# Optimization experiments

Measured on AMD Instinct MI355X. Metric: run time of the kernel, lower is better.

Reference implementation:

```python
import jax, jax.numpy as jnp
import numpy as np

B, N, E, D, NS, H = 32, 4096, 256, 256, 8, 256
N_ITERS, N_SH, N_MESH, MESH_LR = 3, 5, 4, 5.0

def layer_norm(x, scale, bias, eps=1e-5):
    m = jnp.mean(x, axis=-1, keepdims=True)
    v = jnp.var(x, axis=-1, keepdims=True)
    return (x - m) / jnp.sqrt(v + eps) * scale + bias

def sinkhorn(C, a, b, u=None, v=None, n_iters=N_SH):
    # log-domain Sinkhorn with marginals a [B,N], b [B,S]; C [B,N,S]
    log_a, log_b = jnp.log(a), jnp.log(b)
    if u is None:
        u = jnp.zeros_like(a)
    if v is None:
        v = jnp.zeros_like(b)
    K = -C
    for _ in range(n_iters):
        u = log_a - jax.nn.logsumexp(K + v[:, None, :], axis=-1)
        v = log_b - jax.nn.logsumexp(K + u[:, :, None], axis=-2)
    attn = jnp.exp(K + u[:, :, None] + v[:, None, :])
    return attn, u, v

def minimize_entropy_of_sinkhorn(C0, a, b, mesh_lr=MESH_LR, n_mesh=N_MESH):
    # MESH: gradient-descend the cost matrix to minimize entropy of the transport plan
    def ent(C):
        attn, _, _ = sinkhorn(C, a, b)
        return -jnp.sum(attn * jnp.log(attn + 1e-8))
    C = C0
    for _ in range(n_mesh):
        C = C - mesh_lr * jax.grad(ent)(C)
    _, u, v = sinkhorn(C, a, b)
    return C, u, v

def gru_cell(x, h, Wih, Whh, bih, bhh):
    # torch.nn.GRUCell math, gate order (r, z, n)
    gi = x @ Wih.T + bih
    gh = h @ Whh.T + bhh
    ir, iz, inn = jnp.split(gi, 3, axis=-1)
    hr, hz, hn = jnp.split(gh, 3, axis=-1)
    r = jax.nn.sigmoid(ir + hr)
    z = jax.nn.sigmoid(iz + hz)
    n = jnp.tanh(inn + r * hn)
    return (1.0 - z) * n + z * h

def setup_inputs():
    key = jax.random.key(0)
    ks = jax.random.split(key, 16)
    s = 0.02
    return {
        "inputs": jax.random.normal(ks[0], (B, N, E), jnp.float32),
        "slots_init": jax.random.normal(ks[1], (B, NS, D), jnp.float32),
        "ln_in_s": jnp.ones((E,), jnp.float32), "ln_in_b": jnp.zeros((E,), jnp.float32),
        "ln_sl_s": jnp.ones((D,), jnp.float32), "ln_sl_b": jnp.zeros((D,), jnp.float32),
        "ln_mlp_s": jnp.ones((D,), jnp.float32), "ln_mlp_b": jnp.zeros((D,), jnp.float32),
        "Wq": jax.random.normal(ks[2], (D, D), jnp.float32) * s,
        "Wk": jax.random.normal(ks[3], (E, D), jnp.float32) * s,
        "Wv": jax.random.normal(ks[4], (E, D), jnp.float32) * s,
        "wi_W": jax.random.normal(ks[5], (E, 1), jnp.float32) * s, "wi_b": jnp.zeros((1,), jnp.float32),
        "ws_W": jax.random.normal(ks[6], (D, 1), jnp.float32) * s, "ws_b": jnp.zeros((1,), jnp.float32),
        "gru_Wih": jax.random.normal(ks[7], (3 * D, D), jnp.float32) * s,
        "gru_Whh": jax.random.normal(ks[8], (3 * D, D), jnp.float32) * s,
        "gru_bih": jnp.zeros((3 * D,), jnp.float32), "gru_bhh": jnp.zeros((3 * D,), jnp.float32),
        "mlp_W1": jax.random.normal(ks[9], (D, H), jnp.float32) * s, "mlp_b1": jnp.zeros((H,), jnp.float32),
        "mlp_W2": jax.random.normal(ks[10], (H, D), jnp.float32) * s, "mlp_b2": jnp.zeros((D,), jnp.float32),
    }

def reference(inputs, slots_init, ln_in_s, ln_in_b, ln_sl_s, ln_sl_b, ln_mlp_s, ln_mlp_b, Wq, Wk, Wv, wi_W, wi_b, ws_W, ws_b, gru_Wih, gru_Whh, gru_bih, gru_bhh, mlp_W1, mlp_b1, mlp_W2, mlp_b2):
    x = layer_norm(inputs, ln_in_s, ln_in_b)
    k = x @ Wk          # [B,N,D]
    v = x @ Wv          # [B,N,D]
    a = jax.nn.softmax(jnp.squeeze(x @ wi_W, -1) + wi_b[0], axis=-1) * NS  # input marginal [B,N]
    k_sq = jnp.sum(k * k, axis=-1)  # [B,N]

    def step(slots):
        sn = layer_norm(slots, ln_sl_s, ln_sl_b)
        b = jax.nn.softmax(jnp.squeeze(sn @ ws_W, -1) + ws_b[0], axis=-1) * NS  # slot marginal [B,S]
        q = sn @ Wq  # [B,S,D]
        # Euclidean cdist(k, q) via the Gram-matrix identity
        d2 = k_sq[:, :, None] + jnp.sum(q * q, -1)[:, None, :] - 2.0 * jnp.einsum('bnd,bsd->bns', k, q)
        C = jnp.sqrt(jnp.clip(d2, 1e-12))
        C, p, qpot = minimize_entropy_of_sinkhorn(C, a, b)
        attn, _, _ = sinkhorn(C, a, b, u=p, v=qpot)  # warm-started final sinkhorn
        updates = jnp.einsum('bns,bnd->bsd', attn, v)
        h = gru_cell(updates.reshape(-1, D), slots.reshape(-1, D), gru_Wih, gru_Whh, gru_bih, gru_bhh).reshape(B, NS, D)
        hn = layer_norm(h, ln_mlp_s, ln_mlp_b)
        h = h + (jax.nn.relu(hn @ mlp_W1 + mlp_b1) @ mlp_W2 + mlp_b2)
        return h, attn

    slots = slots_init
    attn = None
    for _ in range(N_ITERS - 1):
        slots, attn = step(slots)
    slots = jax.lax.stop_gradient(slots)  # .detach() before final step
    slots, attn = step(slots)
    return slots, jnp.transpose(attn, (0, 2, 1)), slots
```

## Files before the change

### kernel.cpp

```cpp
#include <hip/hip_runtime.h>
#include <hip/hip_bf16.h>

#define B_ 32
#define N_ 4096
#define E_ 256
#define D_ 256
#define NS_ 8
#define LN8 2.0794415416798357f
#define OFF_ATTN 65536
#define OFF_S2   (65536 + 1048576)
#define NSPLIT 8
#define SENT 0xFFFFFFFFu

typedef unsigned short u16;
typedef unsigned short u16x8 __attribute__((ext_vector_type(8)));
typedef __bf16 bf16x8 __attribute__((ext_vector_type(8)));
typedef float floatx4 __attribute__((ext_vector_type(4)));

__device__ __forceinline__ float bf2f(u16 h) {
  unsigned int u = ((unsigned int)h) << 16;
  return __uint_as_float(u);
}
__device__ __forceinline__ u16 f2bf(float f) {
  unsigned int u = __float_as_uint(f);
  unsigned int r = (u + 0x7FFFu + ((u >> 16) & 1u)) >> 16;
  return (u16)r;
}
__device__ __forceinline__ float ldx(const void* p, int i, int dt) {
  return dt ? ((const float*)p)[i] : bf2f(((const u16*)p)[i]);
}
__device__ __forceinline__ void stx(void* p, size_t i, int dt, float v) {
  if (dt) ((float*)p)[i] = v; else ((u16*)p)[i] = f2bf(v);
}
__device__ __forceinline__ float slog(float x) { return __logf(fmaxf(x, 1e-35f)); }
__device__ __forceinline__ float cl(float x) { return fminf(fmaxf(x, -1e30f), 1e30f); }

__device__ __forceinline__ float breduce256(float v, float* red4, int tid) {
  #pragma unroll
  for (int m = 1; m < 64; m <<= 1) v += __shfl_xor(v, m, 64);
  __syncthreads();
  if ((tid & 63) == 0) red4[tid >> 6] = v;
  __syncthreads();
  return red4[0] + red4[1] + red4[2] + red4[3];
}

__device__ __forceinline__ float breduce768(float v, float* red4, int tid) {
  #pragma unroll
  for (int m = 1; m < 64; m <<= 1) v += __shfl_xor(v, m, 64);
  __syncthreads();
  if (tid < 256 && (tid & 63) == 0) red4[tid >> 6] = v;
  __syncthreads();
  return red4[0] + red4[1] + red4[2] + red4[3];
}

__global__ void detect_dtype_kernel(const u16* __restrict__ inp, int* __restrict__ flag) {
  int lane = threadIdx.x & 63;
  int good = 0;
  for (int i = lane; i < 256; i += 64) {
    float x = bf2f(inp[i]);
    float ax = fabsf(x);
    if (x == 0.0f || (ax >= 1e-3f && ax <= 64.0f)) good++;
  }
  #pragma unroll
  for (int m = 1; m < 64; m <<= 1) good += __shfl_xor(good, m, 64);
  if (lane == 0) *flag = (good >= 208) ? 0 : 1;
}


__global__ void tr_kv_kernel(const void* __restrict__ Wk, const void* __restrict__ Wv,
                             u16* __restrict__ WkvT, const int* __restrict__ dtf) {
  const int dt = *dtf;
  int idx = blockIdx.x * 256 + threadIdx.x;
  int half = idx >> 16, i = idx & 65535;
  int r = i >> 8, c = i & 255;
  const void* src = half ? Wv : Wk;
  WkvT[((size_t)(half * 256 + c)) * 256 + r] = f2bf(ldx(src, i, dt));
}

__global__ void cast_w_kernel(const void* __restrict__ Wih, const void* __restrict__ Whh,
                              u16* __restrict__ WihB, u16* __restrict__ WhhB,
                              const int* __restrict__ dtf) {
  const int dt = *dtf;
  int idx = blockIdx.x * 256 + threadIdx.x;
  int half = idx >= 196608;
  int i = idx - (half ? 196608 : 0);
  u16* dst = half ? WhhB : WihB;
  dst[i] = f2bf(ldx(half ? Whh : Wih, i, dt));
}

__global__ void cast_slots_kernel(const void* __restrict__ src, float* __restrict__ dst,
                                  const int* __restrict__ dtf) {
  const int dt = *dtf;
  int i = blockIdx.x * 256 + threadIdx.x;
  dst[i] = ldx(src, i, dt);
}

__global__ __launch_bounds__(256) void ln_stats_kernel(
    const void* __restrict__ inp, const void* __restrict__ lns, const void* __restrict__ lnb,
    const void* __restrict__ wiW, const int* __restrict__ dtf,
    u16* __restrict__ xln, float* __restrict__ logits) {
  const int dt = *dtf;
  int row = blockIdx.x * 4 + (threadIdx.x >> 6);
  int lane = threadIdx.x & 63;
  float xs[4];
  if (dt) {
    float4 h = *(const float4*)((const float*)inp + (size_t)row * E_ + lane * 4);
    xs[0] = h.x; xs[1] = h.y; xs[2] = h.z; xs[3] = h.w;
  } else {
    ushort4 h = *(const ushort4*)((const u16*)inp + (size_t)row * E_ + lane * 4);
    xs[0] = bf2f(h.x); xs[1] = bf2f(h.y); xs[2] = bf2f(h.z); xs[3] = bf2f(h.w);
  }
  float s = xs[0] + xs[1] + xs[2] + xs[3];
  float q = xs[0]*xs[0] + xs[1]*xs[1] + xs[2]*xs[2] + xs[3]*xs[3];
  #pragma unroll
  for (int m = 1; m < 64; m <<= 1) { s += __shfl_xor(s, m, 64); q += __shfl_xor(q, m, 64); }
  float mean = s * (1.0f / E_);
  float var = q * (1.0f / E_) - mean * mean;
  float rstd = rsqrtf(fmaxf(var, 0.0f) + 1e-5f);
  int e = lane * 4;
  float d = 0.0f;
  float xn[4];
  #pragma unroll
  for (int j = 0; j < 4; ++j) {
    xn[j] = (xs[j] - mean) * rstd * ldx(lns, e + j, dt) + ldx(lnb, e + j, dt);
    d += xn[j] * ldx(wiW, e + j, dt);
  }
  ushort4 o;
  o.x = f2bf(xn[0]); o.y = f2bf(xn[1]); o.z = f2bf(xn[2]); o.w = f2bf(xn[3]);
  *(ushort4*)(xln + (size_t)row * E_ + e) = o;
  #pragma unroll
  for (int m = 1; m < 64; m <<= 1) d += __shfl_xor(d, m, 64);
  if (lane == 0) logits[row] = d;
}

__global__ __launch_bounds__(1024) void amarg_kernel(const float* __restrict__ logits,
    float* __restrict__ log_a, float* __restrict__ inva) {
  __shared__ float red[16];
  __shared__ float bcast;
  int b = blockIdx.x, tid = threadIdx.x;
  logits += (size_t)b * N_;
  float l[4];
  #pragma unroll
  for (int i = 0; i < 4; ++i) l[i] = logits[tid + i * 1024];
  float mx = fmaxf(fmaxf(l[0], l[1]), fmaxf(l[2], l[3]));
  #pragma unroll
  for (int m = 1; m < 64; m <<= 1) mx = fmaxf(mx, __shfl_xor(mx, m, 64));
  __syncthreads();
  if ((tid & 63) == 0) red[tid >> 6] = mx;
  __syncthreads();
  if (tid == 0) { float v = red[0]; for (int i = 1; i < 16; ++i) v = fmaxf(v, red[i]); bcast = v; }
  __syncthreads();
  float M = bcast;
  float se = 0.0f;
  #pragma unroll
  for (int i = 0; i < 4; ++i) se += __expf(l[i] - M);
  #pragma unroll
  for (int m = 1; m < 64; m <<= 1) se += __shfl_xor(se, m, 64);
  __syncthreads();
  if ((tid & 63) == 0) red[tid >> 6] = se;
  __syncthreads();
  if (tid == 0) { float v = 0; for (int i = 0; i < 16; ++i) v += red[i]; bcast = v; }
  __syncthreads();
  float lgS = slog(bcast);
  #pragma unroll
  for (int i = 0; i < 4; ++i) {
    float lav = l[i] - M - lgS + LN8;
    log_a[tid + i * 1024] = lav;
    inva[tid + i * 1024] = fminf(__expf(-lav), 1e20f);
  }
}

__global__ __launch_bounds__(256, 2) void gemm_bt_kernel(
    const u16* __restrict__ A, const u16* __restrict__ BT,
    u16* __restrict__ kbf, u16* __restrict__ vbf) {
  __shared__ __align__(16) u16 Als[128 * 32];
  __shared__ __align__(16) u16 Bls[128 * 32];
  int tid = threadIdx.x;
  int m0 = blockIdx.x * 128, n0 = blockIdx.y * 128;
  u16* ob = (n0 < 256) ? kbf : vbf;
  int nb = n0 & 255;
  int w = tid >> 6, lane = tid & 63;
  int wm = (w & 1) * 64, wn = (w >> 1) * 64;
  int fr = lane & 15, kg = lane >> 4;
  floatx4 acc[4][4];
  #pragma unroll
  for (int i = 0; i < 4; ++i)
    #pragma unroll
    for (int j = 0; j < 4; ++j) acc[i][j] = (floatx4){0.f, 0.f, 0.f, 0.f};
  int sm = tid >> 1;
  int sk0 = (tid & 1) * 16;
  const u16* arow = A + (size_t)(m0 + sm) * E_;
  const u16* brow = BT + (size_t)(n0 + sm) * E_;
  for (int kc = 0; kc < E_; kc += 32) {
    #pragma unroll
    for (int j = 0; j < 16; j += 8) {
      int kk = kc + sk0 + j;
      *(u16x8*)&Als[sm * 32 + sk0 + j] = *(const u16x8*)(arow + kk);
      *(u16x8*)&Bls[sm * 32 + sk0 + j] = *(const u16x8*)(brow + kk);
    }
    __syncthreads();
    bf16x8 af[4], bfv[4];
    #pragma unroll
    for (int im = 0; im < 4; ++im) af[im] = *(const bf16x8*)&Als[(wm + im * 16 + fr) * 32 + kg * 8];
    #pragma unroll
    for (int in = 0; in < 4; ++in) bfv[in] = *(const bf16x8*)&Bls[(wn + in * 16 + fr) * 32 + kg * 8];
    #pragma unroll
    for (int im = 0; im < 4; ++im)
      #pragma unroll
      for (int in = 0; in < 4; ++in)
        acc[im][in] = __builtin_amdgcn_mfma_f32_16x16x32_bf16(af[im], bfv[in], acc[im][in], 0, 0, 0);
    __syncthreads();
  }
  #pragma unroll
  for (int im = 0; im < 4; ++im)
    #pragma unroll
    for (int in = 0; in < 4; ++in)
      #pragma unroll
      for (int r = 0; r < 4; ++r) {
        int row = m0 + wm + im * 16 + kg * 4 + r;
        int col = nb + wn + in * 16 + fr;
        ob[(size_t)row * D_ + col] = f2bf(acc[im][in][r]);
      }
}


__global__ __launch_bounds__(256) void s1_kernel(
    const float* __restrict__ slots, const void* __restrict__ lnss, const void* __restrict__ lnsb,
    const void* __restrict__ Wq, const void* __restrict__ wsW, const int* __restrict__ dtf,
    float* __restrict__ qf, float* __restrict__ q_sq, float* __restrict__ logits_b) {
  __shared__ float sn_sh[256];
  __shared__ float red4[4];
  const int dt = *dtf;
  int row = blockIdx.x;
  int tid = threadIdx.x;
  float h = slots[(size_t)row * D_ + tid];
  float sum = breduce256(h, red4, tid);
  float sq = breduce256(h * h, red4, tid);
  float mean = sum * (1.0f / D_), var = sq * (1.0f / D_) - mean * mean;
  float rstd = rsqrtf(fmaxf(var, 0.0f) + 1e-5f);
  float sn = (h - mean) * rstd * ldx(lnss, tid, dt) + ldx(lnsb, tid, dt);
  sn_sh[tid] = sn;
  __syncthreads();
  float acc = 0.0f;
  if (dt) {
    const float* W = (const float*)Wq;
    for (int d = 0; d < 256; ++d) acc += sn_sh[d] * W[d * 256 + tid];
  } else {
    const u16* W = (const u16*)Wq;
    for (int d = 0; d < 256; ++d) acc += sn_sh[d] * bf2f(W[d * 256 + tid]);
  }
  qf[(size_t)row * 256 + tid] = acc;
  float qs = breduce256(acc * acc, red4, tid);
  float lbp = breduce256(sn * ldx(wsW, tid, dt), red4, tid);
  if (tid == 0) { q_sq[row] = qs; logits_b[row] = lbp; }
}

__device__ __forceinline__ float grp_sync_reduce(
    float acc8[8], float (*red)[8],
    unsigned int* gp, int rp, int blkn, int wv, int lane, int tid) {
  #pragma unroll
  for (int m = 1; m < 64; m <<= 1)
    #pragma unroll
    for (int s = 0; s < 8; ++s) acc8[s] += __shfl_xor(acc8[s], m, 64);
  if (lane == 0)
    #pragma unroll
    for (int s = 0; s < 8; ++s) red[wv][s] = acc8[s];
  __syncthreads();
  float x = 0.0f;
  if (tid < 64) {
    float v = red[tid >> 3][tid & 7];
    v += __shfl_xor(v, 8, 64);
    v += __shfl_xor(v, 16, 64);
    v += __shfl_xor(v, 32, 64);
    if (tid < 8)
      __hip_atomic_store(gp + rp * 64 + blkn * 8 + tid, __float_as_uint(v),
                         __ATOMIC_RELAXED, __HIP_MEMORY_SCOPE_AGENT);
    unsigned int u;
    for (;;) {
      u = __hip_atomic_load(gp + rp * 64 + tid, __ATOMIC_RELAXED, __HIP_MEMORY_SCOPE_AGENT);
      if (__all(u != SENT)) break;
      __builtin_amdgcn_s_sleep(1);
    }
    x = __uint_as_float(u);
    x += __shfl_xor(x, 8, 64);
    x += __shfl_xor(x, 16, 64);
    x += __shfl_xor(x, 32, 64);
  }
  return x;
}

__global__ __launch_bounds__(512, 2) void mesh_kernel(
    const u16* __restrict__ kbf, const u16* __restrict__ vbf,
    const float* __restrict__ qf32, const float* __restrict__ qsq_g,
    const float* __restrict__ log_a_g, const float* __restrict__ inva_g,
    const float* __restrict__ logits_b_g, const void* __restrict__ wsb,
    const int* __restrict__ dtf,
    unsigned int* __restrict__ gpart,
    float* __restrict__ updp, void* __restrict__ dout_or_null) {
  const int blkn = blockIdx.x;
  const int b = blockIdx.y;
  const int tid = threadIdx.x;
  const int dt = *dtf;
  const int n = blkn * 512 + tid;

  __shared__ float evP[6][8];
  __shared__ float lb[8], invb[8];
  __shared__ float dv[8];
  __shared__ float red[8][8];
  __shared__ float q_lds[8][256];
  __shared__ float qsq_l[8];
  __shared__ float pv_lds[512][8];

  const float la = log_a_g[(size_t)b * N_ + n];
  const float ia = inva_g[(size_t)b * N_ + n];
  unsigned int* gp = gpart + (size_t)b * 64 * 64;

  {
    const float* qb = qf32 + (size_t)b * 8 * 256;
    #pragma unroll
    for (int i = tid; i < 2048; i += 512) q_lds[i >> 8][i & 255] = qb[i];
    if (tid < 8) {
      qsq_l[tid] = qsq_g[b * 8 + tid];
      float off = ldx(wsb, 0, dt);
      float l[8], M = -1e30f;
      #pragma unroll
      for (int s = 0; s < 8; ++s) { l[s] = logits_b_g[b * 8 + s] + off; M = fmaxf(M, l[s]); }
      float S = 0.0f;
      #pragma unroll
      for (int s = 0; s < 8; ++s) S += __expf(l[s] - M);
      float lgS = slog(S);
      float x = l[tid] - M - lgS + LN8;
      lb[tid] = x; invb[tid] = fminf(__expf(-x), 1e20f);
    }
  }
  __syncthreads();

  float E[8], dK[8], eus[5];
  float eu = 0.0f, dup = 0.0f;
  {
    const u16* kp = kbf + ((size_t)b * N_ + n) * D_;
    float accq[8] = {0, 0, 0, 0, 0, 0, 0, 0};
    float kq = 0.0f;
    for (int kc = 0; kc < 256; kc += 8) {
      u16x8 kv = *(const u16x8*)(kp + kc);
      float kf[8];
      #pragma unroll
      for (int j = 0; j < 8; ++j) { kf[j] = bf2f(kv[j]); kq += kf[j] * kf[j]; }
      #pragma unroll
      for (int s = 0; s < 8; ++s) {
        float4 qa = *(const float4*)&q_lds[s][kc];
        float4 qb2 = *(const float4*)&q_lds[s][kc + 4];
        accq[s] += kf[0] * qa.x + kf[1] * qa.y + kf[2] * qa.z + kf[3] * qa.w
                 + kf[4] * qb2.x + kf[5] * qb2.y + kf[6] * qb2.z + kf[7] * qb2.w;
      }
    }
    #pragma unroll
    for (int s = 0; s < 8; ++s) {
      float d2 = kq + qsq_l[s] - 2.0f * accq[s];
      float Cv = sqrtf(fmaxf(d2, 1e-12f));
      E[s] = __expf(-Cv);
    }
  }

  const int wv = tid >> 6, lane = tid & 63;
  int rp = 0;

  for (int mesh = 0; mesh < 4; ++mesh) {
    if (tid < 8) evP[0][tid] = 1.0f;
    __syncthreads();
    for (int t = 1; t <= 5; ++t) {
      float evp[8];
      #pragma unroll
      for (int s = 0; s < 8; ++s) evp[s] = evP[t - 1][s];
      float su = 0.0f;
      #pragma unroll
      for (int s = 0; s < 8; ++s) su += fminf(E[s] * evp[s], 1e30f);
      float u = la - slog(su);
      eu = fminf(__expf(u), 1e20f);
      eus[t - 1] = eu;
      float acc8[8];
      #pragma unroll
      for (int s = 0; s < 8; ++s) acc8[s] = fminf(E[s] * eu, 1e30f);
      float S = grp_sync_reduce(acc8, red, gp, rp, blkn, wv, lane, tid);
      if (tid < 8) {
        float v = lb[tid] - slog(S);
        evP[t][tid] = fminf(__expf(v), 1e20f);
      }
      ++rp;
      __syncthreads();
    }
    {
      float ev5[8];
      #pragma unroll
      for (int s = 0; s < 8; ++s) ev5[s] = evP[5][s];
      float acc8[8];
      dup = 0.0f;
      #pragma unroll
      for (int s = 0; s < 8; ++s) {
        float t1 = fminf(E[s] * eu, 1e30f);
        float P = fminf(t1 * ev5[s], 1e30f);
        float Pe = P + 1e-8f;
        float g = -(__logf(Pe) + P / Pe) * P;
        dK[s] = g; dup += g; acc8[s] = g;
      }
      float S = grp_sync_reduce(acc8, red, gp, rp, blkn, wv, lane, tid);
      if (tid < 8) dv[tid] = cl(S);
      ++rp;
      __syncthreads();
    }
    for (int t = 5; t >= 1; --t) {
      float evt[8], evtm[8], dvl[8], ibl[8];
      #pragma unroll
      for (int s = 0; s < 8; ++s) { evt[s] = evP[t][s]; evtm[s] = evP[t - 1][s]; dvl[s] = dv[s]; ibl[s] = invb[s]; }
      float eut = eus[t - 1];
      float duv = 0.0f;
      float w8[8];
      #pragma unroll
      for (int s = 0; s < 8; ++s) {
        float a1 = fminf(E[s] * eut, 1e30f);
        float b1 = fminf(a1 * evt[s], 1e30f);
        w8[s] = fminf(b1 * ibl[s], 1e30f);
        duv += cl(dvl[s] * w8[s]);
      }
      float du = ((t == 5) ? dup : 0.0f) - duv;
      float duf = cl(cl(du * ia) * eut);
      float acc8[8];
      #pragma unroll
      for (int s = 0; s < 8; ++s) {
        float ee = fminf(E[s] * evtm[s], 1e30f);
        float zc = cl(ee * duf);
        dK[s] -= cl(dvl[s] * w8[s]) + zc;
        acc8[s] = -zc;
      }
      if (t > 1) {
        float S = grp_sync_reduce(acc8, red, gp, rp, blkn, wv, lane, tid);
        if (tid < 8) dv[tid] = cl(S);
        ++rp;
      }
      __syncthreads();
    }
    #pragma unroll
    for (int s = 0; s < 8; ++s) {
      float dkc = fminf(fmaxf(dK[s], -4.0f), 4.0f);
      float Enew = E[s] * __expf(-5.0f * dkc);
      E[s] = fminf(fmaxf(Enew, 1e-35f), 1e30f);
    }
  }

  if (tid < 8) evP[0][tid] = 1.0f;
  __syncthreads();
  for (int t = 1; t <= 10; ++t) {
    int pc = (t - 1) & 1, cc = t & 1;
    float evp[8];
    #pragma unroll
    for (int s = 0; s < 8; ++s) evp[s] = evP[pc][s];
    float su = 0.0f;
    #pragma unroll
    for (int s = 0; s < 8; ++s) su += fminf(E[s] * evp[s], 1e30f);
    eu = fminf(__expf(la - slog(su)), 1e20f);
    float acc8[8];
    #pragma unroll
    for (int s = 0; s < 8; ++s) acc8[s] = fminf(E[s] * eu, 1e30f);
    float S = grp_sync_reduce(acc8, red, gp, rp, blkn, wv, lane, tid);
    if (tid < 8) {
      float v = lb[tid] - slog(S);
      evP[cc][tid] = fminf(__expf(v), 1e20f);
    }
    ++rp;
    __syncthreads();
  }
  float evf[8];
  #pragma unroll
  for (int s = 0; s < 8; ++s) evf[s] = evP[0][s];
  float pv[8];
  #pragma unroll
  for (int s = 0; s < 8; ++s) {
    float t1 = fminf(E[s] * eu, 1e30f);
    pv[s] = fminf(t1 * evf[s], 1e30f);
  }
  if (dout_or_null) {
    #pragma unroll
    for (int s = 0; s < 8; ++s)
      stx(dout_or_null, (size_t)OFF_ATTN + ((size_t)b * 8 + s) * N_ + n, dt, pv[s]);
  }

  #pragma unroll
  for (int s = 0; s < 8; ++s) pv_lds[tid][s] = pv[s];
  __syncthreads();
  {
    int d = tid & 255, half = tid >> 8;
    const u16* vp = vbf + ((size_t)b * N_ + blkn * 512 + half * 256) * D_ + d;
    float acc[8] = {0, 0, 0, 0, 0, 0, 0, 0};
    for (int i = 0; i < 256; ++i) {
      float vv = bf2f(vp[(size_t)i * D_]);
      float4 a0 = *(const float4*)&pv_lds[half * 256 + i][0];
      float4 a1 = *(const float4*)&pv_lds[half * 256 + i][4];
      acc[0] += a0.x * vv; acc[1] += a0.y * vv; acc[2] += a0.z * vv; acc[3] += a0.w * vv;
      acc[4] += a1.x * vv; acc[5] += a1.y * vv; acc[6] += a1.z * vv; acc[7] += a1.w * vv;
    }
    __syncthreads();
    if (half == 1) {
      #pragma unroll
      for (int s = 0; s < 8; ++s) pv_lds[d][s] = acc[s];
    }
    __syncthreads();
    if (half == 0) {
      #pragma unroll
      for (int s = 0; s < 8; ++s) acc[s] += pv_lds[d][s];
      #pragma unroll
      for (int s = 0; s < 8; ++s)
        updp[(((size_t)b * 8 + blkn) * 8 + s) * D_ + d] = acc[s];
    }
  }
}

__global__ __launch_bounds__(768) void gru_s1_kernel(
    const float* __restrict__ updp, const float* __restrict__ slots_cur,
    const u16* __restrict__ WihB, const u16* __restrict__ WhhB,
    const void* __restrict__ bih, const void* __restrict__ bhh,
    const void* __restrict__ lnms, const void* __restrict__ lnmb,
    const void* __restrict__ W1, const void* __restrict__ b1,
    const void* __restrict__ W2, const void* __restrict__ b2,
    const void* __restrict__ lnss, const void* __restrict__ lnsb,
    const void* __restrict__ Wq, const void* __restrict__ wsW,
    const int* __restrict__ dtf, int do_s1,
    float* __restrict__ slots_next, float* __restrict__ qf,
    float* __restrict__ q_sq, float* __restrict__ logits_b,
    void* __restrict__ dout_or_null) {
  __shared__ float xs[256], hs[256], hns[256], as_[256];
  __shared__ float gi_sh[768], gh_sh[768];
  __shared__ float red4[4];
  const int dt = *dtf;
  int row = blockIdx.x;
  int b = row >> 3, s = row & 7;
  int tid = threadIdx.x;
  if (tid < 256) {
    float x = 0.0f;
    #pragma unroll
    for (int c = 0; c < 8; ++c) x += updp[(((size_t)b * 8 + c) * 8 + s) * D_ + tid];
    xs[tid] = x;
    hs[tid] = slots_cur[(size_t)row * D_ + tid];
  }
  __syncthreads();
  {
    float gi = ldx(bih, tid, dt);
    float gh = ldx(bhh, tid, dt);
    const u16* wi = WihB + (size_t)tid * 256;
    const u16* wh = WhhB + (size_t)tid * 256;
    for (int e = 0; e < 256; e += 8) {
      u16x8 a = *(const u16x8*)(wi + e);
      u16x8 c = *(const u16x8*)(wh + e);
      #pragma unroll
      for (int j = 0; j < 8; ++j) gi += xs[e + j] * bf2f(a[j]);
      #pragma unroll
      for (int j = 0; j < 8; ++j) gh += hs[e + j] * bf2f(c[j]);
    }
    gi_sh[tid] = gi; gh_sh[tid] = gh;
  }
  __syncthreads();
  float h2 = 0.0f;
  if (tid < 256) {
    float r = 1.0f / (1.0f + __expf(-(gi_sh[tid] + gh_sh[tid])));
    float z = 1.0f / (1.0f + __expf(-(gi_sh[256 + tid] + gh_sh[256 + tid])));
    float nn = tanhf(gi_sh[512 + tid] + r * gh_sh[512 + tid]);
    h2 = (1.0f - z) * nn + z * hs[tid];
  }
  float sum = breduce768(h2, red4, tid);
  float sq = breduce768(h2 * h2, red4, tid);
  float mean = sum * (1.0f / D_), var = sq * (1.0f / D_) - mean * mean;
  float rstd = rsqrtf(fmaxf(var, 0.0f) + 1e-5f);
  if (tid < 256) {
    float hn2 = (h2 - mean) * rstd * ldx(lnms, tid, dt) + ldx(lnmb, tid, dt);
    hns[tid] = hn2;
  }
  __syncthreads();
  float o = 0.0f;
  if (tid < 256) {
    float a1 = ldx(b1, tid, dt);
    if (dt) {
      const float* W = (const float*)W1;
      for (int e = 0; e < 256; ++e) a1 += hns[e] * W[e * 256 + tid];
    } else {
      const u16* W = (const u16*)W1;
      for (int e = 0; e < 256; ++e) a1 += hns[e] * bf2f(W[e * 256 + tid]);
    }
    as_[tid] = fmaxf(a1, 0.0f);
  }
  __syncthreads();
  if (tid < 256) {
    o = h2 + ldx(b2, tid, dt);
    if (dt) {
      const float* W = (const float*)W2;
      for (int e = 0; e < 256; ++e) o += as_[e] * W[e * 256 + tid];
    } else {
      const u16* W = (const u16*)W2;
      for (int e = 0; e < 256; ++e) o += as_[e] * bf2f(W[e * 256 + tid]);
    }
    slots_next[(size_t)row * D_ + tid] = o;
    if (dout_or_null) {
      stx(dout_or_null, (size_t)row * D_ + tid, dt, o);
      stx(dout_or_null, (size_t)OFF_S2 + (size_t)row * D_ + tid, dt, o);
    }
  }
  if (do_s1) {
    float sum2 = breduce768(o, red4, tid);
    float sq2 = breduce768(o * o, red4, tid);
    float mean2 = sum2 * (1.0f / D_), var2 = sq2 * (1.0f / D_) - mean2 * mean2;
    float rstd2 = rsqrtf(fmaxf(var2, 0.0f) + 1e-5f);
    float sn = 0.0f;
    __syncthreads();
    if (tid < 256) {
      sn = (o - mean2) * rstd2 * ldx(lnss, tid, dt) + ldx(lnsb, tid, dt);
      xs[tid] = sn;
    }
    __syncthreads();
    float accq = 0.0f;
    if (tid < 256) {
      if (dt) {
        const float* W = (const float*)Wq;
        for (int d = 0; d < 256; ++d) accq += xs[d] * W[d * 256 + tid];
      } else {
        const u16* W = (const u16*)Wq;
        for (int d = 0; d < 256; ++d) accq += xs[d] * bf2f(W[d * 256 + tid]);
      }
      qf[(size_t)row * 256 + tid] = accq;
    }
    float qs = breduce768(accq * accq, red4, tid);
    float lbp = breduce768(tid < 256 ? sn * ldx(wsW, tid, dt) : 0.0f, red4, tid);
    if (tid == 0) { q_sq[row] = qs; logits_b[row] = lbp; }
  }
}


extern "C" void kernel_launch(void* const* d_in, const int* in_sizes, int n_in,
                              void* d_out, int out_size, void* d_ws, size_t ws_size,
                              hipStream_t stream) {
  (void)in_sizes; (void)n_in; (void)out_size;
  const void* inp      = d_in[0];
  const void* slots0   = d_in[1];
  const void* ln_in_s  = d_in[2];
  const void* ln_in_b  = d_in[3];
  const void* ln_sl_s  = d_in[4];
  const void* ln_sl_b  = d_in[5];
  const void* ln_mlp_s = d_in[6];
  const void* ln_mlp_b = d_in[7];
  const void* Wq  = d_in[8];
  const void* Wk  = d_in[9];
  const void* Wv  = d_in[10];
  const void* wiW = d_in[11];
  const void* wsW = d_in[13];
  const void* wsb = d_in[14];
  const void* Wih = d_in[15];
  const void* Whh = d_in[16];
  const void* bih = d_in[17];
  const void* bhh = d_in[18];
  const void* W1  = d_in[19];
  const void* b1  = d_in[20];
  const void* W2  = d_in[21];
  const void* b2  = d_in[22];

  char* ws = (char*)d_ws;
  size_t off = 0;
  auto alloc = [&](size_t bytes) -> void* {
    void* p = ws + off;
    off += (bytes + 255) & ~(size_t)255;
    return p;
  };
  const size_t NR = (size_t)B_ * N_;
  int* dtflag     = (int*)alloc(256);
  float* logits_a = (float*)alloc(NR * 4);
  float* log_a    = (float*)alloc(NR * 4);
  float* inva     = (float*)alloc(NR * 4);
  u16* xln        = (u16*)alloc(NR * E_ * 2);
  u16* kbf        = (u16*)alloc(NR * D_ * 2);
  u16* vbf        = (u16*)alloc(NR * D_ * 2);
  u16* WkvT       = (u16*)alloc((size_t)512 * 256 * 2);
  u16* WihB       = (u16*)alloc(768 * 256 * 2);
  u16* WhhB       = (u16*)alloc(768 * 256 * 2);
  float* qf32     = (float*)alloc((size_t)B_ * 8 * 256 * 4);
  float* q_sq     = (float*)alloc(B_ * 8 * 4);
  float* logits_b = (float*)alloc(B_ * 8 * 4);
  float* updp     = (float*)alloc((size_t)B_ * 8 * 8 * D_ * 4);
  float* slots_a  = (float*)alloc((size_t)B_ * 8 * D_ * 4);
  float* slots_b  = (float*)alloc((size_t)B_ * 8 * D_ * 4);
  unsigned int* gpart = (unsigned int*)alloc((size_t)3 * B_ * 64 * 64 * 4);
  if (ws_size < off) return;

  hipMemsetAsync(gpart, 0xFF, (size_t)3 * B_ * 64 * 64 * 4, stream);
  detect_dtype_kernel<<<1, 64, 0, stream>>>((const u16*)inp, dtflag);

  tr_kv_kernel<<<512, 256, 0, stream>>>(Wk, Wv, WkvT, dtflag);
  cast_w_kernel<<<1536, 256, 0, stream>>>(Wih, Whh, WihB, WhhB, dtflag);
  cast_slots_kernel<<<(B_ * 8 * D_) / 256, 256, 0, stream>>>(slots0, slots_a, dtflag);
  ln_stats_kernel<<<NR / 4, 256, 0, stream>>>(inp, ln_in_s, ln_in_b, wiW, dtflag, xln, logits_a);
  amarg_kernel<<<B_, 1024, 0, stream>>>(logits_a, log_a, inva);
  gemm_bt_kernel<<<dim3(NR / 128, 4), 256, 0, stream>>>(xln, WkvT, kbf, vbf);

  float* scur = slots_a;
  float* snext = slots_b;
  s1_kernel<<<B_ * 8, 256, 0, stream>>>(scur, ln_sl_s, ln_sl_b, Wq, wsW, dtflag, qf32, q_sq, logits_b);
  for (int step = 0; step < 3; ++step) {
    bool last = (step == 2);
    mesh_kernel<<<dim3(NSPLIT, B_), 512, 0, stream>>>(kbf, vbf, qf32, q_sq, log_a, inva,
                                                      logits_b, wsb, dtflag,
                                                      gpart + (size_t)step * B_ * 64 * 64,
                                                      updp, last ? d_out : (void*)nullptr);
    gru_s1_kernel<<<B_ * 8, 768, 0, stream>>>(updp, scur, WihB, WhhB, bih, bhh,
                                              ln_mlp_s, ln_mlp_b, W1, b1, W2, b2,
                                              ln_sl_s, ln_sl_b, Wq, wsW, dtflag, last ? 0 : 1,
                                              snext, qf32, q_sq, logits_b,
                                              last ? d_out : (void*)nullptr);
    float* t = scur; scur = snext; snext = t;
  }
}
```

Baseline: 993.2 us.

## Fold Wk and Wv projections into slot side, drop k/v materialization

Instead of computing and storing k = xln·Wk and v = xln·Wv for all tokens, the mesh kernel now works directly on xln. It uses the projected query q·Wkᵀ for the dot product and a precomputed per-token |k|² from a GEMM kernel that only reduces row norms. The attention-weighted sum over xln is multiplied by Wv afterwards in the GRU kernel. This removes the large k/v GEMM writes and the kbf/vbf reads. In exchange it adds small per-slot matvecs with uncoalesced Wk row reads and changes where bf16 rounding happens.

```diff
diff --git a/kernel.cpp b/kernel.cpp
--- a/kernel.cpp
+++ b/kernel.cpp
@@ -67,14 +67,12 @@
 }
 
 
-__global__ void tr_kv_kernel(const void* __restrict__ Wk, const void* __restrict__ Wv,
-                             u16* __restrict__ WkvT, const int* __restrict__ dtf) {
+__global__ void tr_k_kernel(const void* __restrict__ Wk, u16* __restrict__ WkT,
+                            const int* __restrict__ dtf) {
   const int dt = *dtf;
   int idx = blockIdx.x * 256 + threadIdx.x;
-  int half = idx >> 16, i = idx & 65535;
-  int r = i >> 8, c = i & 255;
-  const void* src = half ? Wv : Wk;
-  WkvT[((size_t)(half * 256 + c)) * 256 + r] = f2bf(ldx(src, i, dt));
+  int r = idx >> 8, c = idx & 255;
+  WkT[(size_t)c * 256 + r] = f2bf(ldx(Wk, idx, dt));
 }
 
 __global__ void cast_w_kernel(const void* __restrict__ Wih, const void* __restrict__ Whh,
@@ -170,64 +168,70 @@
   }
 }
 
-__global__ __launch_bounds__(256, 2) void gemm_bt_kernel(
-    const u16* __restrict__ A, const u16* __restrict__ BT,
-    u16* __restrict__ kbf, u16* __restrict__ vbf) {
+__global__ __launch_bounds__(256, 2) void ksq_kernel(
+    const u16* __restrict__ A, const u16* __restrict__ BT, float* __restrict__ ksq) {
   __shared__ __align__(16) u16 Als[128 * 32];
   __shared__ __align__(16) u16 Bls[128 * 32];
+  __shared__ float rsq[128];
   int tid = threadIdx.x;
-  int m0 = blockIdx.x * 128, n0 = blockIdx.y * 128;
-  u16* ob = (n0 < 256) ? kbf : vbf;
-  int nb = n0 & 255;
+  int m0 = blockIdx.x * 128;
   int w = tid >> 6, lane = tid & 63;
   int wm = (w & 1) * 64, wn = (w >> 1) * 64;
   int fr = lane & 15, kg = lane >> 4;
-  floatx4 acc[4][4];
-  #pragma unroll
-  for (int i = 0; i < 4; ++i)
-    #pragma unroll
-    for (int j = 0; j < 4; ++j) acc[i][j] = (floatx4){0.f, 0.f, 0.f, 0.f};
-  int sm = tid >> 1;
-  int sk0 = (tid & 1) * 16;
+  int sm = tid >> 1, sk0 = (tid & 1) * 16;
+  if (tid < 128) rsq[tid] = 0.0f;
   const u16* arow = A + (size_t)(m0 + sm) * E_;
-  const u16* brow = BT + (size_t)(n0 + sm) * E_;
-  for (int kc = 0; kc < E_; kc += 32) {
-    #pragma unroll
-    for (int j = 0; j < 16; j += 8) {
-      int kk = kc + sk0 + j;
-      *(u16x8*)&Als[sm * 32 + sk0 + j] = *(const u16x8*)(arow + kk);
-      *(u16x8*)&Bls[sm * 32 + sk0 + j] = *(const u16x8*)(brow + kk);
-    }
+  for (int n0 = 0; n0 < 256; n0 += 128) {
+    floatx4 acc[4][4];
+    #pragma unroll
+    for (int i = 0; i < 4; ++i)
+      #pragma unroll
+      for (int j = 0; j < 4; ++j) acc[i][j] = (floatx4){0.f, 0.f, 0.f, 0.f};
+    const u16* brow = BT + (size_t)(n0 + sm) * E_;
     __syncthreads();
-    bf16x8 af[4], bfv[4];
-    #pragma unroll
-    for (int im = 0; im < 4; ++im) af[im] = *(const bf16x8*)&Als[(wm + im * 16 + fr) * 32 + kg * 8];
-    #pragma unroll
-    for (int in = 0; in < 4; ++in) bfv[in] = *(const bf16x8*)&Bls[(wn + in * 16 + fr) * 32 + kg * 8];
+    for (int kc = 0; kc < E_; kc += 32) {
+      #pragma unroll
+      for (int j = 0; j < 16; j += 8) {
+        int kk = kc + sk0 + j;
+        *(u16x8*)&Als[sm * 32 + sk0 + j] = *(const u16x8*)(arow + kk);
+        *(u16x8*)&Bls[sm * 32 + sk0 + j] = *(const u16x8*)(brow + kk);
+      }
+      __syncthreads();
+      bf16x8 af[4], bfv[4];
+      #pragma unroll
+      for (int im = 0; im < 4; ++im) af[im] = *(const bf16x8*)&Als[(wm + im * 16 + fr) * 32 + kg * 8];
+      #pragma unroll
+      for (int in = 0; in < 4; ++in) bfv[in] = *(const bf16x8*)&Bls[(wn + in * 16 + fr) * 32 + kg * 8];
+      #pragma unroll
+      for (int im = 0; im < 4; ++im)
+        #pragma unroll
+        for (int in = 0; in < 4; ++in)
+          acc[im][in] = __builtin_amdgcn_mfma_f32_16x16x32_bf16(af[im], bfv[in], acc[im][in], 0, 0, 0);
+      __syncthreads();
+    }
     #pragma unroll
     for (int im = 0; im < 4; ++im)
       #pragma unroll
-      for (int in = 0; in < 4; ++in)
-        acc[im][in] = __builtin_amdgcn_mfma_f32_16x16x32_bf16(af[im], bfv[in], acc[im][in], 0, 0, 0);
-    __syncthreads();
-  }
-  #pragma unroll
-  for (int im = 0; im < 4; ++im)
-    #pragma unroll
-    for (int in = 0; in < 4; ++in)
-      #pragma unroll
       for (int r = 0; r < 4; ++r) {
-        int row = m0 + wm + im * 16 + kg * 4 + r;
-        int col = nb + wn + in * 16 + fr;
-        ob[(size_t)row * D_ + col] = f2bf(acc[im][in][r]);
-      }
+        float s = acc[im][0][r] * acc[im][0][r] + acc[im][1][r] * acc[im][1][r]
+                + acc[im][2][r] * acc[im][2][r] + acc[im][3][r] * acc[im][3][r];
+        s += __shfl_xor(s, 1, 64);
+        s += __shfl_xor(s, 2, 64);
+        s += __shfl_xor(s, 4, 64);
+        s += __shfl_xor(s, 8, 64);
+        if (fr == 0) atomicAdd(&rsq[wm + im * 16 + kg * 4 + r], s);
+      }
+  }
+  __syncthreads();
+  if (tid < 128) ksq[(size_t)m0 + tid] = rsq[tid];
 }
 
 
 __global__ __launch_bounds__(256) void s1_kernel(
     const float* __restrict__ slots, const void* __restrict__ lnss, const void* __restrict__ lnsb,
-    const void* __restrict__ Wq, const void* __restrict__ wsW, const int* __restrict__ dtf,
-    float* __restrict__ qf, float* __restrict__ q_sq, float* __restrict__ logits_b) {
+    const void* __restrict__ Wq, const void* __restrict__ wsW, const void* __restrict__ Wk,
+    const int* __restrict__ dtf,
+    float* __restrict__ qkbuf, float* __restrict__ q_sq, float* __restrict__ logits_b) {
   __shared__ float sn_sh[256];
   __shared__ float red4[4];
   const int dt = *dtf;
@@ -249,9 +253,14 @@
     const u16* W = (const u16*)Wq;
     for (int d = 0; d < 256; ++d) acc += sn_sh[d] * bf2f(W[d * 256 + tid]);
   }
-  qf[(size_t)row * 256 + tid] = acc;
   float qs = breduce256(acc * acc, red4, tid);
   float lbp = breduce256(sn * ldx(wsW, tid, dt), red4, tid);
+  __syncthreads();
+  sn_sh[tid] = acc;
+  __syncthreads();
+  float qk = 0.0f;
+  for (int d = 0; d < 256; ++d) qk += ldx(Wk, tid * 256 + d, dt) * sn_sh[d];
+  qkbuf[(size_t)row * 256 + tid] = qk;
   if (tid == 0) { q_sq[row] = qs; logits_b[row] = lbp; }
 }
 
@@ -290,8 +299,8 @@
 }
 
 __global__ __launch_bounds__(512, 2) void mesh_kernel(
-    const u16* __restrict__ kbf, const u16* __restrict__ vbf,
-    const float* __restrict__ qf32, const float* __restrict__ qsq_g,
+    const u16* __restrict__ xln, const float* __restrict__ qk32,
+    const float* __restrict__ qsq_g, const float* __restrict__ ksq_g,
     const float* __restrict__ log_a_g, const float* __restrict__ inva_g,
     const float* __restrict__ logits_b_g, const void* __restrict__ wsb,
     const int* __restrict__ dtf,
@@ -316,7 +325,7 @@
   unsigned int* gp = gpart + (size_t)b * 64 * 64;
 
   {
-    const float* qb = qf32 + (size_t)b * 8 * 256;
+    const float* qb = qk32 + (size_t)b * 8 * 256;
     #pragma unroll
     for (int i = tid; i < 2048; i += 512) q_lds[i >> 8][i & 255] = qb[i];
     if (tid < 8) {
@@ -338,14 +347,13 @@
   float E[8], dK[8], eus[5];
   float eu = 0.0f, dup = 0.0f;
   {
-    const u16* kp = kbf + ((size_t)b * N_ + n) * D_;
+    const u16* kp = xln + ((size_t)b * N_ + n) * E_;
     float accq[8] = {0, 0, 0, 0, 0, 0, 0, 0};
-    float kq = 0.0f;
     for (int kc = 0; kc < 256; kc += 8) {
       u16x8 kv = *(const u16x8*)(kp + kc);
       float kf[8];
       #pragma unroll
-      for (int j = 0; j < 8; ++j) { kf[j] = bf2f(kv[j]); kq += kf[j] * kf[j]; }
+      for (int j = 0; j < 8; ++j) kf[j] = bf2f(kv[j]);
       #pragma unroll
       for (int s = 0; s < 8; ++s) {
         float4 qa = *(const float4*)&q_lds[s][kc];
@@ -354,6 +362,7 @@
                  + kf[4] * qb2.x + kf[5] * qb2.y + kf[6] * qb2.z + kf[7] * qb2.w;
       }
     }
+    float kq = ksq_g[(size_t)b * N_ + n];
     #pragma unroll
     for (int s = 0; s < 8; ++s) {
       float d2 = kq + qsq_l[s] - 2.0f * accq[s];
@@ -489,10 +498,10 @@
   __syncthreads();
   {
     int d = tid & 255, half = tid >> 8;
-    const u16* vp = vbf + ((size_t)b * N_ + blkn * 512 + half * 256) * D_ + d;
+    const u16* xp = xln + ((size_t)b * N_ + blkn * 512 + half * 256) * E_ + d;
     float acc[8] = {0, 0, 0, 0, 0, 0, 0, 0};
     for (int i = 0; i < 256; ++i) {
-      float vv = bf2f(vp[(size_t)i * D_]);
+      float vv = bf2f(xp[(size_t)i * E_]);
       float4 a0 = *(const float4*)&pv_lds[half * 256 + i][0];
       float4 a1 = *(const float4*)&pv_lds[half * 256 + i][4];
       acc[0] += a0.x * vv; acc[1] += a0.y * vv; acc[2] += a0.z * vv; acc[3] += a0.w * vv;
@@ -523,11 +532,12 @@
     const void* __restrict__ W2, const void* __restrict__ b2,
     const void* __restrict__ lnss, const void* __restrict__ lnsb,
     const void* __restrict__ Wq, const void* __restrict__ wsW,
+    const void* __restrict__ Wv, const void* __restrict__ Wk,
     const int* __restrict__ dtf, int do_s1,
-    float* __restrict__ slots_next, float* __restrict__ qf,
+    float* __restrict__ slots_next, float* __restrict__ qkbuf,
     float* __restrict__ q_sq, float* __restrict__ logits_b,
     void* __restrict__ dout_or_null) {
-  __shared__ float xs[256], hs[256], hns[256], as_[256];
+  __shared__ float xs[256], hs[256], hns[256], as_[256], ys[256];
   __shared__ float gi_sh[768], gh_sh[768];
   __shared__ float red4[4];
   const int dt = *dtf;
@@ -535,11 +545,17 @@
   int b = row >> 3, s = row & 7;
   int tid = threadIdx.x;
   if (tid < 256) {
+    float y = 0.0f;
+    #pragma unroll
+    for (int c = 0; c < 8; ++c) y += updp[(((size_t)b * 8 + c) * 8 + s) * D_ + tid];
+    ys[tid] = y;
+    hs[tid] = slots_cur[(size_t)row * D_ + tid];
+  }
+  __syncthreads();
+  if (tid < 256) {
     float x = 0.0f;
-    #pragma unroll
-    for (int c = 0; c < 8; ++c) x += updp[(((size_t)b * 8 + c) * 8 + s) * D_ + tid];
+    for (int e = 0; e < 256; ++e) x += ys[e] * ldx(Wv, e * 256 + tid, dt);
     xs[tid] = x;
-    hs[tid] = slots_cur[(size_t)row * D_ + tid];
   }
   __syncthreads();
   {
@@ -623,10 +639,15 @@
         const u16* W = (const u16*)Wq;
         for (int d = 0; d < 256; ++d) accq += xs[d] * bf2f(W[d * 256 + tid]);
       }
-      qf[(size_t)row * 256 + tid] = accq;
+      hs[tid] = accq;
     }
     float qs = breduce768(accq * accq, red4, tid);
     float lbp = breduce768(tid < 256 ? sn * ldx(wsW, tid, dt) : 0.0f, red4, tid);
+    if (tid < 256) {
+      float qk = 0.0f;
+      for (int d = 0; d < 256; ++d) qk += ldx(Wk, tid * 256 + d, dt) * hs[d];
+      qkbuf[(size_t)row * 256 + tid] = qk;
+    }
     if (tid == 0) { q_sq[row] = qs; logits_b[row] = lbp; }
   }
 }
@@ -672,12 +693,11 @@
   float* log_a    = (float*)alloc(NR * 4);
   float* inva     = (float*)alloc(NR * 4);
   u16* xln        = (u16*)alloc(NR * E_ * 2);
-  u16* kbf        = (u16*)alloc(NR * D_ * 2);
-  u16* vbf        = (u16*)alloc(NR * D_ * 2);
-  u16* WkvT       = (u16*)alloc((size_t)512 * 256 * 2);
+  u16* WkT        = (u16*)alloc((size_t)256 * 256 * 2);
   u16* WihB       = (u16*)alloc(768 * 256 * 2);
   u16* WhhB       = (u16*)alloc(768 * 256 * 2);
-  float* qf32     = (float*)alloc((size_t)B_ * 8 * 256 * 4);
+  float* ksq      = (float*)alloc(NR * 4);
+  float* qkbuf    = (float*)alloc((size_t)B_ * 8 * 256 * 4);
   float* q_sq     = (float*)alloc(B_ * 8 * 4);
   float* logits_b = (float*)alloc(B_ * 8 * 4);
   float* updp     = (float*)alloc((size_t)B_ * 8 * 8 * D_ * 4);
@@ -689,26 +709,28 @@
   hipMemsetAsync(gpart, 0xFF, (size_t)3 * B_ * 64 * 64 * 4, stream);
   detect_dtype_kernel<<<1, 64, 0, stream>>>((const u16*)inp, dtflag);
 
-  tr_kv_kernel<<<512, 256, 0, stream>>>(Wk, Wv, WkvT, dtflag);
+  tr_k_kernel<<<256, 256, 0, stream>>>(Wk, WkT, dtflag);
   cast_w_kernel<<<1536, 256, 0, stream>>>(Wih, Whh, WihB, WhhB, dtflag);
   cast_slots_kernel<<<(B_ * 8 * D_) / 256, 256, 0, stream>>>(slots0, slots_a, dtflag);
   ln_stats_kernel<<<NR / 4, 256, 0, stream>>>(inp, ln_in_s, ln_in_b, wiW, dtflag, xln, logits_a);
   amarg_kernel<<<B_, 1024, 0, stream>>>(logits_a, log_a, inva);
-  gemm_bt_kernel<<<dim3(NR / 128, 4), 256, 0, stream>>>(xln, WkvT, kbf, vbf);
+  ksq_kernel<<<NR / 128, 256, 0, stream>>>(xln, WkT, ksq);
 
   float* scur = slots_a;
   float* snext = slots_b;
-  s1_kernel<<<B_ * 8, 256, 0, stream>>>(scur, ln_sl_s, ln_sl_b, Wq, wsW, dtflag, qf32, q_sq, logits_b);
+  s1_kernel<<<B_ * 8, 256, 0, stream>>>(scur, ln_sl_s, ln_sl_b, Wq, wsW, Wk, dtflag,
+                                        qkbuf, q_sq, logits_b);
   for (int step = 0; step < 3; ++step) {
     bool last = (step == 2);
-    mesh_kernel<<<dim3(NSPLIT, B_), 512, 0, stream>>>(kbf, vbf, qf32, q_sq, log_a, inva,
+    mesh_kernel<<<dim3(NSPLIT, B_), 512, 0, stream>>>(xln, qkbuf, q_sq, ksq, log_a, inva,
                                                       logits_b, wsb, dtflag,
                                                       gpart + (size_t)step * B_ * 64 * 64,
                                                       updp, last ? d_out : (void*)nullptr);
     gru_s1_kernel<<<B_ * 8, 768, 0, stream>>>(updp, scur, WihB, WhhB, bih, bhh,
                                               ln_mlp_s, ln_mlp_b, W1, b1, W2, b2,
-                                              ln_sl_s, ln_sl_b, Wq, wsW, dtflag, last ? 0 : 1,
-                                              snext, qf32, q_sq, logits_b,
+                                              ln_sl_s, ln_sl_b, Wq, wsW, Wv, Wk,
+                                              dtflag, last ? 0 : 1,
+                                              snext, qkbuf, q_sq, logits_b,
                                               last ? d_out : (void*)nullptr);
     float* t = scur; scur = snext; snext = t;
   }
```

Result: slower. 1.120 ms (+12.8%).
